# Kernel optimization log

Measured on AMD Instinct MI355X. Metric: run time of the kernel, lower is better.

The kernel has to match this reference:

```python
import jax, jax.numpy as jnp
import numpy as np

N_NODES = 50000   # batch_size * num_nodes
N_EDGES = 800000
D_IN = 128
D_OUT = 128


def setup_inputs() -> dict:
    key = jax.random.key(0)
    k1, k2, k3, k4 = jax.random.split(key, 4)
    x = jax.random.normal(k1, (N_NODES, D_IN), dtype=jnp.float32)
    edge_index = jax.random.randint(k2, (2, N_EDGES), 0, N_NODES, dtype=jnp.int64)
    W = jax.random.normal(k3, (D_OUT, D_IN), dtype=jnp.float32) * (1.0 / np.sqrt(D_IN))
    b = jax.random.normal(k4, (D_OUT,), dtype=jnp.float32) * 0.01
    return {"x": x, "edge_index": edge_index, "batch_size": 50, "num_nodes": 1000, "W": W, "b": b}


def reference(x, edge_index, batch_size, num_nodes, W, b):
    dim_size = batch_size * num_nodes
    row, col = edge_index[0], edge_index[1]
    # gather messages and segment-mean aggregate over destination rows
    msgs = x[col]                                   # [E, D_IN]
    summed = jax.ops.segment_sum(msgs, row, num_segments=dim_size)      # [N, D_IN]
    counts = jax.ops.segment_sum(jnp.ones((row.shape[0],), dtype=x.dtype), row,
                                 num_segments=dim_size)                 # [N]
    mean = summed / jnp.maximum(counts, 1.0)[:, None]                   # 0 for empty rows
    # linear projection (torch Linear: y = x @ W.T + b)
    return mean @ W.T + b
```

## Files before the change

### kernel.cpp

```cpp
#include <hip/hip_runtime.h>

#define D 128
#define BSHIFT 6
#define BCAP 1536
#define EPB_A 2048

typedef unsigned short ushort_t;
typedef unsigned int uint_t;

__device__ __forceinline__ bool eidx_is64(const int* eidx) {
    int lane = threadIdx.x & 63;
    int probe = eidx[2 * lane + 1];
    return __ballot(probe != 0) == 0ULL;
}

__device__ __forceinline__ uint_t f2bf(float f) {
    union { float f; uint_t i; } v; v.f = f;
    return (v.i + 0x7fffu + ((v.i >> 16) & 1u)) >> 16;
}
__device__ __forceinline__ float bf_lo(uint_t w) {
    union { uint_t i; float f; } v; v.i = w << 16; return v.f;
}
__device__ __forceinline__ float bf_hi(uint_t w) {
    union { uint_t i; float f; } v; v.i = w & 0xffff0000u; return v.f;
}

__global__ __launch_bounds__(256) void bucketA_kernel(
    const int* __restrict__ eidx, int* __restrict__ gcur,
    int* __restrict__ bucket, int E, int NBUK) {
    __shared__ int lhist[1024];
    __shared__ int lbase[1024];
    bool is64 = eidx_is64(eidx);
    int t = threadIdx.x;
    for (int i = t; i < NBUK; i += 256) lhist[i] = 0;
    __syncthreads();

    int e0 = blockIdx.x * EPB_A;
    int e1 = min(e0 + EPB_A, E);
    for (int e = e0 + t; e < e1; e += 256) {
        int r = is64 ? eidx[2 * e] : eidx[e];
        atomicAdd(&lhist[r >> BSHIFT], 1);
    }
    __syncthreads();
    for (int i = t; i < NBUK; i += 256) {
        int h = lhist[i];
        lbase[i] = (h > 0) ? atomicAdd(&gcur[i], h) : 0;
        lhist[i] = 0;
    }
    __syncthreads();
    for (int e = e0 + t; e < e1; e += 256) {
        int r, c;
        if (is64) { r = eidx[2 * e]; c = eidx[2 * E + 2 * e]; }
        else      { r = eidx[e];     c = eidx[E + e]; }
        int b = r >> BSHIFT;
        int p = atomicAdd(&lhist[b], 1);
        int idx = lbase[b] + p;
        if (idx < BCAP) bucket[b * BCAP + idx] = ((r & 63) << 24) | c;
    }
}

__global__ __launch_bounds__(256) void prep_kernel(
    const int* __restrict__ gcur, const int* __restrict__ bucket,
    int* __restrict__ elist, int* __restrict__ cnt,
    int* __restrict__ start, int N, int NBUK,
    const float* __restrict__ x, uint_t* __restrict__ xb, int total8) {
    __shared__ int lcnt[64], lpos[64], lstart[64];
    int t = threadIdx.x;

    if ((int)blockIdx.x >= NBUK) {
        int cb = blockIdx.x - NBUK;
        int i = cb * 256 + t;
        if (xb != nullptr && i < total8) {
            const float4* p = (const float4*)(x + (size_t)i * 8);
            float4 a = p[0], b = p[1];
            uint4 o;
            o.x = f2bf(a.x) | (f2bf(a.y) << 16);
            o.y = f2bf(a.z) | (f2bf(a.w) << 16);
            o.z = f2bf(b.x) | (f2bf(b.y) << 16);
            o.w = f2bf(b.z) | (f2bf(b.w) << 16);
            *(uint4*)(xb + (size_t)i * 4) = o;
        }
        if (xb != nullptr && cb == 0 && t < 16) {
            uint4 z; z.x = 0u; z.y = 0u; z.z = 0u; z.w = 0u;
            ((uint4*)(xb + (size_t)N * (D / 2)))[t] = z;
        }
        return;
    }

    int b = blockIdx.x;
    if (t < 64) { lcnt[t] = 0; lpos[t] = 0; }
    __syncthreads();
    int tot = min(gcur[b], BCAP);
    const int* bp = bucket + (size_t)b * BCAP;
    for (int i = t; i < tot; i += 256)
        atomicAdd(&lcnt[bp[i] >> 24], 1);
    __syncthreads();
    if (t == 0) {
        int run = 0;
        #pragma unroll
        for (int i = 0; i < 64; ++i) {
            lstart[i] = run;
            run += (lcnt[i] + 7) & ~7;
        }
    }
    __syncthreads();
    for (int i = t; i < tot; i += 256) {
        int v = bp[i];
        int rl = v >> 24;
        int p = atomicAdd(&lpos[rl], 1);
        int idx = lstart[rl] + p;
        if (idx < BCAP) elist[(size_t)b * BCAP + idx] = v & 0xFFFFFF;
    }
    if (t < 64) {
        int gr = (b << BSHIFT) + t;
        int c0 = lcnt[t];
        int pe = (c0 + 7) & ~7;
        for (int p = c0; p < pe; ++p) {
            int idx = lstart[t] + p;
            if (idx < BCAP) elist[(size_t)b * BCAP + idx] = N;
        }
        if (gr < N) { cnt[gr] = c0; start[gr] = b * BCAP + lstart[t]; }
    }
}

#define GATHER8(CA, CB)                                                       \
    {                                                                         \
        uint4 g0 = *(const uint4*)(xs + (size_t)(CA).x * D);                  \
        uint4 g1 = *(const uint4*)(xs + (size_t)(CA).y * D);                  \
        uint4 g2 = *(const uint4*)(xs + (size_t)(CA).z * D);                  \
        uint4 g3 = *(const uint4*)(xs + (size_t)(CA).w * D);                  \
        uint4 g4 = *(const uint4*)(xs + (size_t)(CB).x * D);                  \
        uint4 g5 = *(const uint4*)(xs + (size_t)(CB).y * D);                  \
        uint4 g6 = *(const uint4*)(xs + (size_t)(CB).z * D);                  \
        uint4 g7 = *(const uint4*)(xs + (size_t)(CB).w * D);                  \
        a0 += ((bf_lo(g0.x) + bf_lo(g1.x)) + (bf_lo(g2.x) + bf_lo(g3.x)))     \
            + ((bf_lo(g4.x) + bf_lo(g5.x)) + (bf_lo(g6.x) + bf_lo(g7.x)));    \
        a1 += ((bf_hi(g0.x) + bf_hi(g1.x)) + (bf_hi(g2.x) + bf_hi(g3.x)))     \
            + ((bf_hi(g4.x) + bf_hi(g5.x)) + (bf_hi(g6.x) + bf_hi(g7.x)));    \
        a2 += ((bf_lo(g0.y) + bf_lo(g1.y)) + (bf_lo(g2.y) + bf_lo(g3.y)))     \
            + ((bf_lo(g4.y) + bf_lo(g5.y)) + (bf_lo(g6.y) + bf_lo(g7.y)));    \
        a3 += ((bf_hi(g0.y) + bf_hi(g1.y)) + (bf_hi(g2.y) + bf_hi(g3.y)))     \
            + ((bf_hi(g4.y) + bf_hi(g5.y)) + (bf_hi(g6.y) + bf_hi(g7.y)));    \
        a4 += ((bf_lo(g0.z) + bf_lo(g1.z)) + (bf_lo(g2.z) + bf_lo(g3.z)))     \
            + ((bf_lo(g4.z) + bf_lo(g5.z)) + (bf_lo(g6.z) + bf_lo(g7.z)));    \
        a5 += ((bf_hi(g0.z) + bf_hi(g1.z)) + (bf_hi(g2.z) + bf_hi(g3.z)))     \
            + ((bf_hi(g4.z) + bf_hi(g5.z)) + (bf_hi(g6.z) + bf_hi(g7.z)));    \
        a6 += ((bf_lo(g0.w) + bf_lo(g1.w)) + (bf_lo(g2.w) + bf_lo(g3.w)))     \
            + ((bf_lo(g4.w) + bf_lo(g5.w)) + (bf_lo(g6.w) + bf_lo(g7.w)));    \
        a7 += ((bf_hi(g0.w) + bf_hi(g1.w)) + (bf_hi(g2.w) + bf_hi(g3.w)))     \
            + ((bf_hi(g4.w) + bf_hi(g5.w)) + (bf_hi(g6.w) + bf_hi(g7.w)));    \
    }

__global__ __launch_bounds__(256, 6) void fused_bf_kernel(
    const ushort_t* __restrict__ xb, const int* __restrict__ elist,
    const int* __restrict__ cnt, const int* __restrict__ start,
    const float* __restrict__ W, const float* __restrict__ bias,
    float* __restrict__ out, int N) {
    __shared__ float sT[128 * 32];
    __shared__ float wc[16 * 132];
    int t = threadIdx.x;
    int lane = t & 63, wave = t >> 6;
    int qr = lane >> 4, sl = lane & 15;
    int nbase = blockIdx.x * 32;
    int rot = (sl & 7) * 4;
    const ushort_t* xs = xb + 8 * sl;

    #pragma unroll
    for (int quad = 0; quad < 2; ++quad) {
        int n = wave * 8 + quad * 4 + qr;
        int gn = nbase + n;
        int nr  = (gn < N) ? cnt[gn]   : 0;
        int beg = (gn < N) ? start[gn] : 0;
        int nr8 = (nr + 7) & ~7;
        int mn = nr8;
        mn = min(mn, __shfl_xor(mn, 16));
        mn = min(mn, __shfl_xor(mn, 32));
        float a0 = 0.f, a1 = 0.f, a2 = 0.f, a3 = 0.f;
        float a4 = 0.f, a5 = 0.f, a6 = 0.f, a7 = 0.f;
        const int* ep = elist + beg;
        int4 cA, cB;
        if (nr8 > 0) { cA = *(const int4*)ep; cB = *(const int4*)(ep + 4); }
        int i = 0;
        for (; i < mn; ) {
            int ni = i + 8;
            int4 nA2, nB2;
            if (ni < nr8) {
                nA2 = *(const int4*)(ep + ni);
                nB2 = *(const int4*)(ep + ni + 4);
            }
            GATHER8(cA, cB)
            cA = nA2; cB = nB2; i = ni;
        }
        for (; i < nr8; i += 8) {
            int4 dA = *(const int4*)(ep + i);
            int4 dB = *(const int4*)(ep + i + 4);
            GATHER8(dA, dB)
        }
        float inv = (nr > 0) ? 1.0f / (float)nr : 0.0f;
        int col = (n + rot) & 31;
        int k0 = 8 * sl;
        sT[((k0 + 0) << 5) + col] = a0 * inv;
        sT[((k0 + 1) << 5) + col] = a1 * inv;
        sT[((k0 + 2) << 5) + col] = a2 * inv;
        sT[((k0 + 3) << 5) + col] = a3 * inv;
        sT[((k0 + 4) << 5) + col] = a4 * inv;
        sT[((k0 + 5) << 5) + col] = a5 * inv;
        sT[((k0 + 6) << 5) + col] = a6 * inv;
        sT[((k0 + 7) << 5) + col] = a7 * inv;
    }

    int jg = t & 31, ng = t >> 5;
    int j0 = jg * 4, n0 = ng * 4;
    float acc[4][4] = {};

    for (int kc = 0; kc < 8; ++kc) {
        __syncthreads();
        #pragma unroll
        for (int i = 0; i < 8; ++i) {
            int idx = t + i * 256;
            int j = idx >> 4, kk = idx & 15;
            wc[kk * 132 + j] = W[j * D + kc * 16 + kk];
        }
        __syncthreads();

        #pragma unroll
        for (int kk = 0; kk < 16; ++kk) {
            int k = kc * 16 + kk;
            int scol = (n0 + ((k >> 3) & 7) * 4) & 31;
            float4 s4 = *(const float4*)(sT + (k << 5) + scol);
            float4 w4 = *(const float4*)(wc + kk * 132 + j0);
            acc[0][0] = fmaf(s4.x, w4.x, acc[0][0]); acc[0][1] = fmaf(s4.x, w4.y, acc[0][1]);
            acc[0][2] = fmaf(s4.x, w4.z, acc[0][2]); acc[0][3] = fmaf(s4.x, w4.w, acc[0][3]);
            acc[1][0] = fmaf(s4.y, w4.x, acc[1][0]); acc[1][1] = fmaf(s4.y, w4.y, acc[1][1]);
            acc[1][2] = fmaf(s4.y, w4.z, acc[1][2]); acc[1][3] = fmaf(s4.y, w4.w, acc[1][3]);
            acc[2][0] = fmaf(s4.z, w4.x, acc[2][0]); acc[2][1] = fmaf(s4.z, w4.y, acc[2][1]);
            acc[2][2] = fmaf(s4.z, w4.z, acc[2][2]); acc[2][3] = fmaf(s4.z, w4.w, acc[2][3]);
            acc[3][0] = fmaf(s4.w, w4.x, acc[3][0]); acc[3][1] = fmaf(s4.w, w4.y, acc[3][1]);
            acc[3][2] = fmaf(s4.w, w4.z, acc[3][2]); acc[3][3] = fmaf(s4.w, w4.w, acc[3][3]);
        }
    }

    float4 b4 = *(const float4*)(bias + j0);
    #pragma unroll
    for (int i = 0; i < 4; ++i) {
        int gn = nbase + n0 + i;
        if (gn >= N) continue;
        float4 o;
        o.x = acc[i][0] + b4.x;
        o.y = acc[i][1] + b4.y;
        o.z = acc[i][2] + b4.z;
        o.w = acc[i][3] + b4.w;
        *(float4*)(out + (size_t)gn * D + j0) = o;
    }
}

__global__ __launch_bounds__(256, 6) void fused_kernel(
    const float* __restrict__ x, const int* __restrict__ elist,
    const int* __restrict__ cnt, const int* __restrict__ start,
    const float* __restrict__ W, const float* __restrict__ bias,
    float* __restrict__ out, int N) {
    __shared__ float sT[128 * 36];
    __shared__ float wc[16 * 132];
    int t = threadIdx.x;
    int lane = t & 63, wave = t >> 6;
    int half = lane >> 5, sl = lane & 31;
    int nbase = blockIdx.x * 32;

    #pragma unroll
    for (int pair = 0; pair < 4; ++pair) {
        int n = wave * 8 + pair * 2 + half;
        int gn = nbase + n;
        int nr  = (gn < N) ? cnt[gn]   : 0;
        int beg = (gn < N) ? start[gn] : 0;
        int nro  = __shfl(nr, lane ^ 32);
        int both = min(nr, nro);
        float ax = 0.f, ay = 0.f, az = 0.f, aw = 0.f;
        int i = 0;
        for (; i + 8 <= both; i += 8) {
            int4 cA = *(const int4*)(elist + beg + i);
            int4 cB = *(const int4*)(elist + beg + i + 4);
            float4 v0 = *(const float4*)(x + (size_t)cA.x * D + 4 * sl);
            float4 v1 = *(const float4*)(x + (size_t)cA.y * D + 4 * sl);
            float4 v2 = *(const float4*)(x + (size_t)cA.z * D + 4 * sl);
            float4 v3 = *(const float4*)(x + (size_t)cA.w * D + 4 * sl);
            float4 v4 = *(const float4*)(x + (size_t)cB.x * D + 4 * sl);
            float4 v5 = *(const float4*)(x + (size_t)cB.y * D + 4 * sl);
            float4 v6 = *(const float4*)(x + (size_t)cB.z * D + 4 * sl);
            float4 v7 = *(const float4*)(x + (size_t)cB.w * D + 4 * sl);
            ax += ((v0.x + v1.x) + (v2.x + v3.x)) + ((v4.x + v5.x) + (v6.x + v7.x));
            ay += ((v0.y + v1.y) + (v2.y + v3.y)) + ((v4.y + v5.y) + (v6.y + v7.y));
            az += ((v0.z + v1.z) + (v2.z + v3.z)) + ((v4.z + v5.z) + (v6.z + v7.z));
            aw += ((v0.w + v1.w) + (v2.w + v3.w)) + ((v4.w + v5.w) + (v6.w + v7.w));
        }
        for (; i < nr; ++i) {
            int c0 = elist[beg + i];
            float4 v = *(const float4*)(x + (size_t)c0 * D + 4 * sl);
            ax += v.x; ay += v.y; az += v.z; aw += v.w;
        }
        float inv = (nr > 0) ? 1.0f / (float)nr : 0.0f;
        int k0 = 4 * sl;
        sT[(k0 + 0) * 36 + n] = ax * inv;
        sT[(k0 + 1) * 36 + n] = ay * inv;
        sT[(k0 + 2) * 36 + n] = az * inv;
        sT[(k0 + 3) * 36 + n] = aw * inv;
    }

    int jg = t & 31, ng = t >> 5;
    int j0 = jg * 4, n0 = ng * 4;
    float acc[4][4] = {};
    for (int kc = 0; kc < 8; ++kc) {
        __syncthreads();
        #pragma unroll
        for (int i = 0; i < 8; ++i) {
            int idx = t + i * 256;
            int j = idx >> 4, kk = idx & 15;
            wc[kk * 132 + j] = W[j * D + kc * 16 + kk];
        }
        __syncthreads();
        #pragma unroll
        for (int kk = 0; kk < 16; ++kk) {
            int k = kc * 16 + kk;
            float4 s4 = *(const float4*)(sT + k * 36 + n0);
            float4 w4 = *(const float4*)(wc + kk * 132 + j0);
            acc[0][0] = fmaf(s4.x, w4.x, acc[0][0]); acc[0][1] = fmaf(s4.x, w4.y, acc[0][1]);
            acc[0][2] = fmaf(s4.x, w4.z, acc[0][2]); acc[0][3] = fmaf(s4.x, w4.w, acc[0][3]);
            acc[1][0] = fmaf(s4.y, w4.x, acc[1][0]); acc[1][1] = fmaf(s4.y, w4.y, acc[1][1]);
            acc[1][2] = fmaf(s4.y, w4.z, acc[1][2]); acc[1][3] = fmaf(s4.y, w4.w, acc[1][3]);
            acc[2][0] = fmaf(s4.z, w4.x, acc[2][0]); acc[2][1] = fmaf(s4.z, w4.y, acc[2][1]);
            acc[2][2] = fmaf(s4.z, w4.z, acc[2][2]); acc[2][3] = fmaf(s4.z, w4.w, acc[2][3]);
            acc[3][0] = fmaf(s4.w, w4.x, acc[3][0]); acc[3][1] = fmaf(s4.w, w4.y, acc[3][1]);
            acc[3][2] = fmaf(s4.w, w4.z, acc[3][2]); acc[3][3] = fmaf(s4.w, w4.w, acc[3][3]);
        }
    }
    float4 b4 = *(const float4*)(bias + j0);
    #pragma unroll
    for (int i = 0; i < 4; ++i) {
        int gn = nbase + n0 + i;
        if (gn >= N) continue;
        float4 o;
        o.x = acc[i][0] + b4.x;
        o.y = acc[i][1] + b4.y;
        o.z = acc[i][2] + b4.z;
        o.w = acc[i][3] + b4.w;
        *(float4*)(out + (size_t)gn * D + j0) = o;
    }
}

__global__ __launch_bounds__(256) void scatter_kernel(
    const float* __restrict__ x, const int* __restrict__ eidx,
    float* summed, float* __restrict__ counts, int E) {
    int t = blockIdx.x * 256 + threadIdx.x;
    int lane = threadIdx.x & 63;
    bool is64 = eidx_is64(eidx);
    int e = t >> 6;
    if (e >= E) return;
    int d = lane * 2;
    int r, c;
    if (is64) { r = eidx[2 * e]; c = eidx[2 * E + 2 * e]; }
    else      { r = eidx[e];     c = eidx[E + e]; }
    float2 v = *(const float2*)(x + (size_t)c * D + d);
    float* dst = summed + (size_t)r * D + d;
    atomicAdd(dst, v.x);
    atomicAdd(dst + 1, v.y);
    if (lane == 0) atomicAdd(counts + r, 1.0f);
}

__global__ __launch_bounds__(256) void divide_kernel(
    float* __restrict__ sums, const float* __restrict__ counts, int N) {
    int g = blockIdx.x * 256 + threadIdx.x;
    int r = g >> 6, lane = g & 63;
    if (r >= N) return;
    float inv = 1.0f / fmaxf(counts[r], 1.0f);
    float2* p = (float2*)(sums + (size_t)r * D + 2 * lane);
    float2 v = *p;
    v.x *= inv; v.y *= inv;
    *p = v;
}

__global__ __launch_bounds__(256) void gemm_kernel(
    float* inout, const float* __restrict__ W,
    const float* __restrict__ bias, int N) {
    __shared__ float sT[128 * 36];
    __shared__ float wc[32 * 132];
    int t = threadIdx.x;
    int nbase = blockIdx.x * 32;
    #pragma unroll
    for (int i = 0; i < 16; ++i) {
        int idx = t + i * 256;
        int n = idx >> 7, k = idx & 127;
        int gn = nbase + n;
        sT[k * 36 + n] = (gn < N) ? inout[(size_t)gn * D + k] : 0.0f;
    }
    int jg = t & 31, ng = t >> 5;
    int j0 = jg * 4, n0 = ng * 4;
    float acc[4][4] = {};
    for (int kc = 0; kc < 4; ++kc) {
        __syncthreads();
        #pragma unroll
        for (int i = 0; i < 16; ++i) {
            int idx = t + i * 256;
            int j = idx >> 5, kk = idx & 31;
            wc[kk * 132 + j] = W[j * D + kc * 32 + kk];
        }
        __syncthreads();
        #pragma unroll 8
        for (int kk = 0; kk < 32; ++kk) {
            int k = kc * 32 + kk;
            float4 s4 = *(const float4*)(sT + k * 36 + n0);
            float4 w4 = *(const float4*)(wc + kk * 132 + j0);
            acc[0][0] = fmaf(s4.x, w4.x, acc[0][0]); acc[0][1] = fmaf(s4.x, w4.y, acc[0][1]);
            acc[0][2] = fmaf(s4.x, w4.z, acc[0][2]); acc[0][3] = fmaf(s4.x, w4.w, acc[0][3]);
            acc[1][0] = fmaf(s4.y, w4.x, acc[1][0]); acc[1][1] = fmaf(s4.y, w4.y, acc[1][1]);
            acc[1][2] = fmaf(s4.y, w4.z, acc[1][2]); acc[1][3] = fmaf(s4.y, w4.w, acc[1][3]);
            acc[2][0] = fmaf(s4.z, w4.x, acc[2][0]); acc[2][1] = fmaf(s4.z, w4.y, acc[2][1]);
            acc[2][2] = fmaf(s4.z, w4.z, acc[2][2]); acc[2][3] = fmaf(s4.z, w4.w, acc[2][3]);
            acc[3][0] = fmaf(s4.w, w4.x, acc[3][0]); acc[3][1] = fmaf(s4.w, w4.y, acc[3][1]);
            acc[3][2] = fmaf(s4.w, w4.z, acc[3][2]); acc[3][3] = fmaf(s4.w, w4.w, acc[3][3]);
        }
    }
    float4 b4 = *(const float4*)(bias + j0);
    #pragma unroll
    for (int i = 0; i < 4; ++i) {
        int gn = nbase + n0 + i;
        if (gn >= N) continue;
        float4 o;
        o.x = acc[i][0] + b4.x;
        o.y = acc[i][1] + b4.y;
        o.z = acc[i][2] + b4.z;
        o.w = acc[i][3] + b4.w;
        *(float4*)(inout + (size_t)gn * D + j0) = o;
    }
}

extern "C" void kernel_launch(void* const* d_in, const int* in_sizes, int n_in,
                              void* d_out, int out_size, void* d_ws, size_t ws_size,
                              hipStream_t stream) {
    const float* x = (const float*)d_in[0];
    const int* eidx = (const int*)d_in[1];
    const float* W = (const float*)d_in[4];
    const float* b = (const float*)d_in[5];
    float* out = (float*)d_out;

    int N = in_sizes[0] / D;
    int E = in_sizes[1] / 2;
    int NBUK = (N + 63) >> BSHIFT;
    int fb = (N + 31) / 32;
    int ab = (E + EPB_A - 1) / EPB_A;

    size_t o0 = 0;
    size_t o_gc = o0;  o0 += ((size_t)NBUK * 4 + 255) & ~255ULL;
    size_t o_cn = o0;  o0 += ((size_t)N * 4 + 255) & ~255ULL;
    size_t o_st = o0;  o0 += ((size_t)N * 4 + 255) & ~255ULL;
    size_t o_bk = o0;  o0 += (size_t)NBUK * BCAP * 4;
    size_t o_el = o0;  o0 += (size_t)NBUK * BCAP * 4;
    size_t base_need = o0;
    size_t o_xb = o0;  size_t bf_need = o0 + (size_t)(N + 1) * D * 2;

    bool cap_ok = (N <= 65536) && ((size_t)NBUK * BCAP >= (size_t)E);

    int cvb = (N * D / 8 + 255) / 256;

    if (cap_ok && ws_size >= bf_need) {
        char* ws = (char*)d_ws;
        int*      gcur  = (int*)(ws + o_gc);
        int*      cnt   = (int*)(ws + o_cn);
        int*      start = (int*)(ws + o_st);
        int*      bkt   = (int*)(ws + o_bk);
        int*      elist = (int*)(ws + o_el);
        ushort_t* xb    = (ushort_t*)(ws + o_xb);

        hipMemsetAsync(gcur, 0, (size_t)NBUK * 4, stream);
        bucketA_kernel<<<ab, 256, 0, stream>>>(eidx, gcur, bkt, E, NBUK);
        prep_kernel<<<NBUK + cvb, 256, 0, stream>>>(
            gcur, bkt, elist, cnt, start, N, NBUK, x, (uint_t*)xb, N * D / 8);
        fused_bf_kernel<<<fb, 256, 0, stream>>>(xb, elist, cnt, start, W, b, out, N);
    } else if (cap_ok && ws_size >= base_need) {
        char* ws = (char*)d_ws;
        int* gcur  = (int*)(ws + o_gc);
        int* cnt   = (int*)(ws + o_cn);
        int* start = (int*)(ws + o_st);
        int* bkt   = (int*)(ws + o_bk);
        int* elist = (int*)(ws + o_el);

        hipMemsetAsync(gcur, 0, (size_t)NBUK * 4, stream);
        bucketA_kernel<<<ab, 256, 0, stream>>>(eidx, gcur, bkt, E, NBUK);
        prep_kernel<<<NBUK, 256, 0, stream>>>(
            gcur, bkt, elist, cnt, start, N, NBUK, nullptr, nullptr, 0);
        fused_kernel<<<fb, 256, 0, stream>>>(x, elist, cnt, start, W, b, out, N);
    } else {
        float* counts = (float*)d_ws;
        hipMemsetAsync(d_out, 0, (size_t)N * D * sizeof(float), stream);
        hipMemsetAsync(d_ws, 0, (size_t)N * sizeof(float), stream);
        int sb = (E * 64 + 255) / 256;
        scatter_kernel<<<sb, 256, 0, stream>>>(x, eidx, out, counts, E);
        int db = (N * 64 + 255) / 256;
        divide_kernel<<<db, 256, 0, stream>>>(out, counts, N);
        gemm_kernel<<<fb, 256, 0, stream>>>(out, W, b, N);
    }
}
```

Before: 169.3 us.

## Replace scalar FP32 projection GEMM with bf16 MFMA using pre-converted weights

The per-block 32x128x128 projection in the fused kernel now uses bf16 MFMA 16x16x32 instructions instead of a scalar FMA loop over FP32 shared-memory tiles. The mean rows are packed to bf16 in LDS, and W is converted to bf16 once in extra blocks of the prep kernel, so the fused kernel reads bf16 W fragments straight from global memory. This removes the per-chunk W staging, its barriers, and most of the FMA ALU work. In exchange it rounds the mean and W to bf16, which adds error, and it writes the output as scalar strided stores.

```diff
diff --git a/kernel.cpp b/kernel.cpp
--- a/kernel.cpp
+++ b/kernel.cpp
@@ -7,6 +7,8 @@
 
 typedef unsigned short ushort_t;
 typedef unsigned int uint_t;
+typedef __attribute__((ext_vector_type(8))) short short8_t;
+typedef __attribute__((ext_vector_type(4))) float f32x4_t;
 
 __device__ __forceinline__ bool eidx_is64(const int* eidx) {
     int lane = threadIdx.x & 63;
@@ -63,26 +65,42 @@
     const int* __restrict__ gcur, const int* __restrict__ bucket,
     int* __restrict__ elist, int* __restrict__ cnt,
     int* __restrict__ start, int N, int NBUK,
-    const float* __restrict__ x, uint_t* __restrict__ xb, int total8) {
+    const float* __restrict__ x, uint_t* __restrict__ xb, int total8, int cvb,
+    const float* __restrict__ Wsrc, uint_t* __restrict__ wb) {
     __shared__ int lcnt[64], lpos[64], lstart[64];
     int t = threadIdx.x;
 
     if ((int)blockIdx.x >= NBUK) {
+        if (xb == nullptr) return;
         int cb = blockIdx.x - NBUK;
-        int i = cb * 256 + t;
-        if (xb != nullptr && i < total8) {
-            const float4* p = (const float4*)(x + (size_t)i * 8);
-            float4 a = p[0], b = p[1];
-            uint4 o;
-            o.x = f2bf(a.x) | (f2bf(a.y) << 16);
-            o.y = f2bf(a.z) | (f2bf(a.w) << 16);
-            o.z = f2bf(b.x) | (f2bf(b.y) << 16);
-            o.w = f2bf(b.z) | (f2bf(b.w) << 16);
-            *(uint4*)(xb + (size_t)i * 4) = o;
-        }
-        if (xb != nullptr && cb == 0 && t < 16) {
-            uint4 z; z.x = 0u; z.y = 0u; z.z = 0u; z.w = 0u;
-            ((uint4*)(xb + (size_t)N * (D / 2)))[t] = z;
+        if (cb < cvb) {
+            int i = cb * 256 + t;
+            if (i < total8) {
+                const float4* p = (const float4*)(x + (size_t)i * 8);
+                float4 a = p[0], b = p[1];
+                uint4 o;
+                o.x = f2bf(a.x) | (f2bf(a.y) << 16);
+                o.y = f2bf(a.z) | (f2bf(a.w) << 16);
+                o.z = f2bf(b.x) | (f2bf(b.y) << 16);
+                o.w = f2bf(b.z) | (f2bf(b.w) << 16);
+                *(uint4*)(xb + (size_t)i * 4) = o;
+            }
+            if (cb == 0 && t < 16) {
+                uint4 z; z.x = 0u; z.y = 0u; z.z = 0u; z.w = 0u;
+                ((uint4*)(xb + (size_t)N * (D / 2)))[t] = z;
+            }
+        } else {
+            int i = (cb - cvb) * 256 + t;
+            if (i < D * D / 8) {
+                const float4* p = (const float4*)(Wsrc + (size_t)i * 8);
+                float4 a = p[0], b = p[1];
+                uint4 o;
+                o.x = f2bf(a.x) | (f2bf(a.y) << 16);
+                o.y = f2bf(a.z) | (f2bf(a.w) << 16);
+                o.z = f2bf(b.x) | (f2bf(b.y) << 16);
+                o.w = f2bf(b.z) | (f2bf(b.w) << 16);
+                *(uint4*)(wb + (size_t)i * 4) = o;
+            }
         }
         return;
     }
@@ -154,15 +172,13 @@
 __global__ __launch_bounds__(256, 6) void fused_bf_kernel(
     const ushort_t* __restrict__ xb, const int* __restrict__ elist,
     const int* __restrict__ cnt, const int* __restrict__ start,
-    const float* __restrict__ W, const float* __restrict__ bias,
+    const ushort_t* __restrict__ Wb, const float* __restrict__ bias,
     float* __restrict__ out, int N) {
-    __shared__ float sT[128 * 32];
-    __shared__ float wc[16 * 132];
+    __shared__ ushort_t sA[32 * 136];
     int t = threadIdx.x;
     int lane = t & 63, wave = t >> 6;
     int qr = lane >> 4, sl = lane & 15;
     int nbase = blockIdx.x * 32;
-    int rot = (sl & 7) * 4;
     const ushort_t* xs = xb + 8 * sl;
 
     #pragma unroll
@@ -197,60 +213,44 @@
             GATHER8(dA, dB)
         }
         float inv = (nr > 0) ? 1.0f / (float)nr : 0.0f;
-        int col = (n + rot) & 31;
-        int k0 = 8 * sl;
-        sT[((k0 + 0) << 5) + col] = a0 * inv;
-        sT[((k0 + 1) << 5) + col] = a1 * inv;
-        sT[((k0 + 2) << 5) + col] = a2 * inv;
-        sT[((k0 + 3) << 5) + col] = a3 * inv;
-        sT[((k0 + 4) << 5) + col] = a4 * inv;
-        sT[((k0 + 5) << 5) + col] = a5 * inv;
-        sT[((k0 + 6) << 5) + col] = a6 * inv;
-        sT[((k0 + 7) << 5) + col] = a7 * inv;
-    }
-
-    int jg = t & 31, ng = t >> 5;
-    int j0 = jg * 4, n0 = ng * 4;
-    float acc[4][4] = {};
-
-    for (int kc = 0; kc < 8; ++kc) {
-        __syncthreads();
-        #pragma unroll
-        for (int i = 0; i < 8; ++i) {
-            int idx = t + i * 256;
-            int j = idx >> 4, kk = idx & 15;
-            wc[kk * 132 + j] = W[j * D + kc * 16 + kk];
-        }
-        __syncthreads();
-
-        #pragma unroll
-        for (int kk = 0; kk < 16; ++kk) {
-            int k = kc * 16 + kk;
-            int scol = (n0 + ((k >> 3) & 7) * 4) & 31;
-            float4 s4 = *(const float4*)(sT + (k << 5) + scol);
-            float4 w4 = *(const float4*)(wc + kk * 132 + j0);
-            acc[0][0] = fmaf(s4.x, w4.x, acc[0][0]); acc[0][1] = fmaf(s4.x, w4.y, acc[0][1]);
-            acc[0][2] = fmaf(s4.x, w4.z, acc[0][2]); acc[0][3] = fmaf(s4.x, w4.w, acc[0][3]);
-            acc[1][0] = fmaf(s4.y, w4.x, acc[1][0]); acc[1][1] = fmaf(s4.y, w4.y, acc[1][1]);
-            acc[1][2] = fmaf(s4.y, w4.z, acc[1][2]); acc[1][3] = fmaf(s4.y, w4.w, acc[1][3]);
-            acc[2][0] = fmaf(s4.z, w4.x, acc[2][0]); acc[2][1] = fmaf(s4.z, w4.y, acc[2][1]);
-            acc[2][2] = fmaf(s4.z, w4.z, acc[2][2]); acc[2][3] = fmaf(s4.z, w4.w, acc[2][3]);
-            acc[3][0] = fmaf(s4.w, w4.x, acc[3][0]); acc[3][1] = fmaf(s4.w, w4.y, acc[3][1]);
-            acc[3][2] = fmaf(s4.w, w4.z, acc[3][2]); acc[3][3] = fmaf(s4.w, w4.w, acc[3][3]);
-        }
-    }
-
-    float4 b4 = *(const float4*)(bias + j0);
-    #pragma unroll
-    for (int i = 0; i < 4; ++i) {
-        int gn = nbase + n0 + i;
-        if (gn >= N) continue;
-        float4 o;
-        o.x = acc[i][0] + b4.x;
-        o.y = acc[i][1] + b4.y;
-        o.z = acc[i][2] + b4.z;
-        o.w = acc[i][3] + b4.w;
-        *(float4*)(out + (size_t)gn * D + j0) = o;
+        uint4 pk;
+        pk.x = f2bf(a0 * inv) | (f2bf(a1 * inv) << 16);
+        pk.y = f2bf(a2 * inv) | (f2bf(a3 * inv) << 16);
+        pk.z = f2bf(a4 * inv) | (f2bf(a5 * inv) << 16);
+        pk.w = f2bf(a6 * inv) | (f2bf(a7 * inv) << 16);
+        *(uint4*)(sA + n * 136 + 8 * sl) = pk;
+    }
+    __syncthreads();
+
+    {
+        int rt = wave & 1, jgrp = wave >> 1;
+        int ml = lane & 15, kh = lane >> 4;
+        short8_t afr[4];
+        #pragma unroll
+        for (int ks = 0; ks < 4; ++ks)
+            afr[ks] = *(const short8_t*)(sA + (rt * 16 + ml) * 136 + ks * 32 + kh * 8);
+        f32x4_t acc[4];
+        #pragma unroll
+        for (int q = 0; q < 4; ++q) acc[q] = (f32x4_t){0.f, 0.f, 0.f, 0.f};
+        #pragma unroll
+        for (int q = 0; q < 4; ++q) {
+            int j = (jgrp * 4 + q) * 16 + ml;
+            #pragma unroll
+            for (int ks = 0; ks < 4; ++ks) {
+                short8_t bfr = *(const short8_t*)(Wb + (size_t)j * D + ks * 32 + kh * 8);
+                acc[q] = __builtin_amdgcn_mfma_f32_16x16x32_bf16(afr[ks], bfr, acc[q], 0, 0, 0);
+            }
+        }
+        #pragma unroll
+        for (int q = 0; q < 4; ++q) {
+            int j = (jgrp * 4 + q) * 16 + ml;
+            float bj = bias[j];
+            #pragma unroll
+            for (int r = 0; r < 4; ++r) {
+                int gn = nbase + rt * 16 + kh * 4 + r;
+                if (gn < N) out[(size_t)gn * D + j] = acc[q][r] + bj;
+            }
+        }
     }
 }
 
@@ -454,11 +454,13 @@
     size_t o_bk = o0;  o0 += (size_t)NBUK * BCAP * 4;
     size_t o_el = o0;  o0 += (size_t)NBUK * BCAP * 4;
     size_t base_need = o0;
-    size_t o_xb = o0;  size_t bf_need = o0 + (size_t)(N + 1) * D * 2;
+    size_t o_xb = o0;  o0 += (((size_t)(N + 1) * D * 2) + 255) & ~255ULL;
+    size_t o_wb = o0;  size_t bf_need = o0 + (size_t)D * D * 2;
 
     bool cap_ok = (N <= 65536) && ((size_t)NBUK * BCAP >= (size_t)E);
 
     int cvb = (N * D / 8 + 255) / 256;
+    int wvb = (D * D / 8 + 255) / 256;
 
     if (cap_ok && ws_size >= bf_need) {
         char* ws = (char*)d_ws;
@@ -468,12 +470,14 @@
         int*      bkt   = (int*)(ws + o_bk);
         int*      elist = (int*)(ws + o_el);
         ushort_t* xb    = (ushort_t*)(ws + o_xb);
+        ushort_t* wb    = (ushort_t*)(ws + o_wb);
 
         hipMemsetAsync(gcur, 0, (size_t)NBUK * 4, stream);
         bucketA_kernel<<<ab, 256, 0, stream>>>(eidx, gcur, bkt, E, NBUK);
-        prep_kernel<<<NBUK + cvb, 256, 0, stream>>>(
-            gcur, bkt, elist, cnt, start, N, NBUK, x, (uint_t*)xb, N * D / 8);
-        fused_bf_kernel<<<fb, 256, 0, stream>>>(xb, elist, cnt, start, W, b, out, N);
+        prep_kernel<<<NBUK + cvb + wvb, 256, 0, stream>>>(
+            gcur, bkt, elist, cnt, start, N, NBUK,
+            x, (uint_t*)xb, N * D / 8, cvb, W, (uint_t*)wb);
+        fused_bf_kernel<<<fb, 256, 0, stream>>>(xb, elist, cnt, start, wb, b, out, N);
     } else if (cap_ok && ws_size >= base_need) {
         char* ws = (char*)d_ws;
         int* gcur  = (int*)(ws + o_gc);
@@ -485,7 +489,8 @@
         hipMemsetAsync(gcur, 0, (size_t)NBUK * 4, stream);
         bucketA_kernel<<<ab, 256, 0, stream>>>(eidx, gcur, bkt, E, NBUK);
         prep_kernel<<<NBUK, 256, 0, stream>>>(
-            gcur, bkt, elist, cnt, start, N, NBUK, nullptr, nullptr, 0);
+            gcur, bkt, elist, cnt, start, N, NBUK,
+            nullptr, nullptr, 0, 0, nullptr, nullptr);
         fused_kernel<<<fb, 256, 0, stream>>>(x, elist, cnt, start, W, b, out, N);
     } else {
         float* counts = (float*)d_ws;
```

Result: faster. 164.5 us (-2.8%).
